# Performance work log

Measured on AMD Instinct MI355X. Metric: run time of the kernel, lower is better.

## Reference

```python
import jax, jax.numpy as jnp
import numpy as np

WS = 16         # window size
NH = 16         # num heads
EPS = 1e-6


def _ln(x):
    m = jnp.mean(x, axis=-1, keepdims=True)
    v = jnp.var(x, axis=-1, keepdims=True)
    return (x - m) * jax.lax.rsqrt(v + EPS)


def _modulate(x, shift, scale):
    return x * (1.0 + scale[:, None, :]) + shift[:, None, :]


def setup_inputs() -> dict:
    key = jax.random.key(0)
    ks = jax.random.split(key, 14)
    D, HD = 1024, 64
    s = 0.02
    return {
        'x': jax.random.normal(ks[0], (4, 4096, D), jnp.float32),
        'c': jax.random.normal(ks[1], (4, D), jnp.float32),
        'qkv_w': jax.random.normal(ks[2], (3 * D, D), jnp.float32) * s,
        'qkv_b': jax.random.normal(ks[3], (3 * D,), jnp.float32) * s,
        'proj_w': jax.random.normal(ks[4], (D, D), jnp.float32) * s,
        'proj_b': jax.random.normal(ks[5], (D,), jnp.float32) * s,
        'rel_pos_h': jax.random.normal(ks[6], (2 * WS - 1, HD), jnp.float32) * s,
        'rel_pos_w': jax.random.normal(ks[7], (2 * WS - 1, HD), jnp.float32) * s,
        'adaLN_w': jax.random.normal(ks[8], (6 * D, D), jnp.float32) * s,
        'adaLN_b': jax.random.normal(ks[9], (6 * D,), jnp.float32) * s,
        'fc1_w': jax.random.normal(ks[10], (4 * D, D), jnp.float32) * s,
        'fc1_b': jax.random.normal(ks[11], (4 * D,), jnp.float32) * s,
        'fc2_w': jax.random.normal(ks[12], (D, 4 * D), jnp.float32) * s,
        'fc2_b': jax.random.normal(ks[13], (D,), jnp.float32) * s,
    }


def _window_attention(x, qkv_w, qkv_b, proj_w, proj_b, rel_pos_h, rel_pos_w):
    # x: [N, T, D] with T = h*w, h = w = sqrt(T)
    N, T, D = x.shape
    h = w = int(round(T ** 0.5))
    nwh, nww = h // WS, w // WS  # grid divides evenly -> no padding
    hd = D // NH
    scale = hd ** -0.5

    # window partition: [N, h, w, D] -> [B, WS, WS, D], B = N*nwh*nww
    xw = x.reshape(N, nwh, WS, nww, WS, D).transpose(0, 1, 3, 2, 4, 5)
    xw = xw.reshape(N * nwh * nww, WS, WS, D)
    B = xw.shape[0]
    L = WS * WS

    qkv = (xw.reshape(B, L, D) @ qkv_w.T + qkv_b)  # [B, L, 3D]
    qkv = qkv.reshape(B, L, 3, NH, hd).transpose(2, 0, 3, 1, 4)  # [3, B, NH, L, hd]
    qkv = qkv.reshape(3, B * NH, L, hd)
    q, k, v = qkv[0], qkv[1], qkv[2]

    attn = jnp.einsum('bqc,bkc->bqk', q * scale, k)  # [B*NH, L, L]

    # decomposed relative position bias (q_size == k_size == WS)
    coords = jnp.arange(WS)
    rel_idx = coords[:, None] - coords[None, :] + (WS - 1)  # [WS, WS]
    Rh = rel_pos_h[rel_idx]  # [WS(q_h), WS(k_h), hd]
    Rw = rel_pos_w[rel_idx]  # [WS(q_w), WS(k_w), hd]
    rq = q.reshape(B * NH, WS, WS, hd)
    rel_h = jnp.einsum('bhwc,hkc->bhwk', rq, Rh)  # [B*NH, WS, WS, WS(kh)]
    rel_w = jnp.einsum('bhwc,wkc->bhwk', rq, Rw)  # [B*NH, WS, WS, WS(kw)]
    attn = (attn.reshape(B * NH, WS, WS, WS, WS)
            + rel_h[:, :, :, :, None]
            + rel_w[:, :, :, None, :]).reshape(B * NH, L, L)

    probs = jax.nn.softmax(attn, axis=-1)
    out = probs @ v  # [B*NH, L, hd]
    out = out.reshape(B, NH, WS, WS, hd).transpose(0, 2, 3, 1, 4).reshape(B, WS, WS, D)
    out = out @ proj_w.T + proj_b

    # window unpartition: [B, WS, WS, D] -> [N, T, D]
    out = out.reshape(N, nwh, nww, WS, WS, D).transpose(0, 1, 3, 2, 4, 5)
    return out.reshape(N, T, D)


def reference(x, c, qkv_w, qkv_b, proj_w, proj_b, rel_pos_h, rel_pos_w,
              adaLN_w, adaLN_b, fc1_w, fc1_b, fc2_w, fc2_b):
    D = x.shape[-1]
    mod = jax.nn.silu(c) @ adaLN_w.T + adaLN_b  # [N, 6D]
    sh_msa, sc_msa, g_msa, sh_mlp, sc_mlp, g_mlp = jnp.split(mod, 6, axis=1)

    a_in = _modulate(_ln(x), sh_msa, sc_msa)
    a_out = _window_attention(a_in, qkv_w, qkv_b, proj_w, proj_b, rel_pos_h, rel_pos_w)
    x = x + g_msa[:, None, :] * a_out

    m_in = _modulate(_ln(x), sh_mlp, sc_mlp)
    hdn = jax.nn.gelu(m_in @ fc1_w.T + fc1_b, approximate=True)
    m_out = hdn @ fc2_w.T + fc2_b
    x = x + g_mlp[:, None, :] * m_out
    return x
```

## Files before the change

### kernel.cpp

```cpp
#include <hip/hip_runtime.h>
#include <cstdint>
#include <cstddef>


typedef float  f32x4    __attribute__((ext_vector_type(4)));
typedef __bf16 bf16x8_t __attribute__((ext_vector_type(8)));
typedef __bf16 bf16x4_t __attribute__((ext_vector_type(4)));

#define DEV __device__ __forceinline__

DEV void gload_lds16(const void* g, void* l) {
    auto gp = (const uint32_t __attribute__((address_space(1)))*)(uintptr_t)g;
    auto lp = (uint32_t __attribute__((address_space(3)))*)(uint32_t)(uintptr_t)l;
    __builtin_amdgcn_global_load_lds(gp, lp, 16, 0, 0);
}

DEV bf16x8_t lds_frag(const __bf16* base, int row, int chunk, int row_elems) {
    return *(const bf16x8_t*)(base + row * row_elems + ((chunk ^ (row & 7)) << 3));
}

DEV bf16x8_t p_frag(const __bf16* base, int row, int chunk) {
    return *(const bf16x8_t*)(base + row * 32 + ((chunk ^ ((row >> 1) & 3)) << 3));
}

DEV int vt_addr(int d, int k) {
    return d * 64 + ((((k >> 3) ^ (d & 7) ^ ((d >> 3) & 7)) << 3) | (k & 7));
}

DEV float gelu_tanh(float v) {
    float u = 0.7978845608028654f * (v + 0.044715f * v * v * v);
    float e = __expf(2.f * u);
    float th = 1.f - 2.f / (e + 1.f);
    return 0.5f * v * (1.f + th);
}

DEV int win2tok(int r) {
    int nb = r >> 12, wi = (r >> 8) & 15, l = r & 255;
    return (nb << 12) + (wi >> 2) * 1024 + (l >> 4) * 64 + (wi & 3) * 16 + (l & 15);
}

__global__ void silu_k(const float* __restrict__ c, float* __restrict__ o, int n) {
    int i = blockIdx.x * 256 + threadIdx.x;
    if (i < n) { float v = c[i]; o[i] = v / (1.f + __expf(-v)); }
}

__global__ void zero_k(float* o, int n) {
    int i = blockIdx.x * 256 + threadIdx.x;
    if (i < n) o[i] = 0.f;
}

__global__ void conv_bf16(const float* __restrict__ s, __bf16* __restrict__ d, int n4) {
    int i = blockIdx.x * 256 + threadIdx.x;
    if (i < n4) {
        float4 v = ((const float4*)s)[i];
        bf16x4_t o; o[0] = (__bf16)v.x; o[1] = (__bf16)v.y; o[2] = (__bf16)v.z; o[3] = (__bf16)v.w;
        ((bf16x4_t*)d)[i] = o;
    }
}

__global__ __launch_bounds__(256)
void mod_gemv(const float* __restrict__ sc, const float* __restrict__ w,
              const float* __restrict__ b, float* __restrict__ mod) {
    int o = (blockIdx.x << 2) + (threadIdx.x >> 6);
    int lane = threadIdx.x & 63;
    int n = o / 6144, col = o % 6144;
    const float4* wr = (const float4*)(w + (size_t)col * 1024);
    const float4* sr = (const float4*)(sc + n * 1024);
    float acc = 0.f;
    #pragma unroll 4
    for (int i = lane; i < 256; i += 64) {
        float4 a = wr[i], x = sr[i];
        acc += a.x * x.x + a.y * x.y + a.z * x.z + a.w * x.w;
    }
    #pragma unroll
    for (int m = 1; m < 64; m <<= 1) acc += __shfl_xor(acc, m);
    if (lane == 0) mod[o] = acc + b[col];
}

__global__ __launch_bounds__(256)
void ln_mod_k(const float* __restrict__ src, const float* __restrict__ mod,
              int sh_off, int sc_off, __bf16* __restrict__ out, int permute, int r0) {
    int rl = blockIdx.x;
    int r = rl + r0;
    int nb = r >> 12;
    int t = permute ? win2tok(r) : r;
    float4 v = ((const float4*)(src + (size_t)t * 1024))[threadIdx.x];
    float s  = v.x + v.y + v.z + v.w;
    float sq = v.x * v.x + v.y * v.y + v.z * v.z + v.w * v.w;
    #pragma unroll
    for (int m = 1; m < 64; m <<= 1) { s += __shfl_xor(s, m); sq += __shfl_xor(sq, m); }
    __shared__ float ps[4], pq[4];
    int wv = threadIdx.x >> 6, ln = threadIdx.x & 63;
    if (ln == 0) { ps[wv] = s; pq[wv] = sq; }
    __syncthreads();
    s  = ps[0] + ps[1] + ps[2] + ps[3];
    sq = pq[0] + pq[1] + pq[2] + pq[3];
    float mean = s * (1.f / 1024.f);
    float var  = sq * (1.f / 1024.f) - mean * mean;
    float rstd = rsqrtf(var + 1e-6f);
    int c = threadIdx.x << 2;
    const float* mrow = mod + nb * 6144;
    float4 scv = *(const float4*)(mrow + sc_off + c);
    float4 shv = *(const float4*)(mrow + sh_off + c);
    bf16x4_t o;
    o[0] = (__bf16)((v.x - mean) * rstd * (1.f + scv.x) + shv.x);
    o[1] = (__bf16)((v.y - mean) * rstd * (1.f + scv.y) + shv.y);
    o[2] = (__bf16)((v.z - mean) * rstd * (1.f + scv.z) + shv.z);
    o[3] = (__bf16)((v.w - mean) * rstd * (1.f + scv.w) + shv.w);
    *(bf16x4_t*)(out + (size_t)rl * 1024 + c) = o;
}

template <int PM, int PN>
DEV void mfma16(f32x4 (&acc)[8][4], bf16x8_t (&fa)[4][2], bf16x8_t (&fb)[2][2][2]) {
    #pragma unroll
    for (int ks = 0; ks < 2; ++ks)
        #pragma unroll
        for (int mi = 0; mi < 4; ++mi)
            #pragma unroll
            for (int nn = 0; nn < 2; ++nn)
                acc[PM * 4 + mi][PN * 2 + nn] = __builtin_amdgcn_mfma_f32_16x16x32_bf16(
                    fa[mi][ks], fb[PN][nn][ks], acc[PM * 4 + mi][PN * 2 + nn], 0, 0, 0);
}

#define GBAR  __builtin_amdgcn_s_barrier()
#define PRIO1 __builtin_amdgcn_s_setprio(1)
#define PRIO0 __builtin_amdgcn_s_setprio(0)

template <int EPI>
__global__ __launch_bounds__(512)
void gemm256(const __bf16* __restrict__ A, const __bf16* __restrict__ B,
             const float* __restrict__ bias, void* __restrict__ Cout,
             const float* __restrict__ extra, const float* __restrict__ mod,
             int N, int K, int r0, int gx) {
    extern __shared__ __align__(16) char smem[];
    __bf16* lA = (__bf16*)smem;
    __bf16* lB = lA + 2 * 16384;
    const int tid = threadIdx.x, lane = tid & 63, wv = tid >> 6;
    const int wr = wv >> 2, wc = wv & 3;

    const int nwg = gridDim.x;
    const int qq = nwg >> 3, rr8 = nwg & 7;
    const int xcd = blockIdx.x & 7, pos = blockIdx.x >> 3;
    const int nid = (xcd < rr8 ? xcd * (qq + 1) : rr8 * (qq + 1) + (xcd - rr8) * qq) + pos;
    const int bm = (nid / gx) << 8, bn = (nid % gx) << 8;

    f32x4 acc[8][4];
    const f32x4 z4 = {0.f, 0.f, 0.f, 0.f};
    #pragma unroll
    for (int i = 0; i < 8; ++i)
        #pragma unroll
        for (int j = 0; j < 4; ++j) acc[i][j] = z4;

    bf16x8_t fa[4][2], fb[2][2][2];

    const int l8  = lane >> 3;
    const int gc8 = ((lane & 7) ^ l8) << 3;
    const int rbw = ((wv & 3) << 3) + ((wv >> 2) << 6);
    const __bf16* gA0 = A + (size_t)(bm +       (wv << 3) + l8) * K + gc8;
    const __bf16* gA1 = A + (size_t)(bm + 128 + (wv << 3) + l8) * K + gc8;
    const __bf16* gA2 = A + (size_t)(bm +  64 + (wv << 3) + l8) * K + gc8;
    const __bf16* gA3 = A + (size_t)(bm + 192 + (wv << 3) + l8) * K + gc8;
    const __bf16* gB0 = B + (size_t)(bn +       rbw + l8) * K + gc8;
    const __bf16* gB1 = B + (size_t)(bn + 128 + rbw + l8) * K + gc8;
    const __bf16* gB2 = B + (size_t)(bn +  32 + rbw + l8) * K + gc8;
    const __bf16* gB3 = B + (size_t)(bn + 160 + rbw + l8) * K + gc8;
    const int dA0 = (wv << 3) * 64, dA1 = (128 + (wv << 3)) * 64;
    const int dA2 = (64 + (wv << 3)) * 64, dA3 = (192 + (wv << 3)) * 64;
    const int dB0 = rbw * 64, dB1 = (128 + rbw) * 64;
    const int dB2 = (32 + rbw) * 64, dB3 = (160 + rbw) * 64;

    auto stageAll = [&](int be2) {
        gload_lds16(gA0, lA + be2 + dA0); gload_lds16(gA1, lA + be2 + dA1);
        gload_lds16(gB0, lB + be2 + dB0); gload_lds16(gB1, lB + be2 + dB1);
        gload_lds16(gB2, lB + be2 + dB2); gload_lds16(gB3, lB + be2 + dB3);
        gload_lds16(gA2, lA + be2 + dA2); gload_lds16(gA3, lA + be2 + dA3);
        gA0 += 64; gA1 += 64; gA2 += 64; gA3 += 64;
        gB0 += 64; gB1 += 64; gB2 += 64; gB3 += 64;
    };

    const int swzb = (lane >> 4) ^ (lane & 7);
    const __bf16* aR0 = lA + (wr << 13) + ((lane & 15) << 6) + (swzb << 3);
    const __bf16* aR1 = lA + (wr << 13) + ((lane & 15) << 6) + ((swzb ^ 4) << 3);
    const __bf16* bR0 = lB + (wc << 12) + ((lane & 15) << 6) + (swzb << 3);
    const __bf16* bR1 = lB + (wc << 12) + ((lane & 15) << 6) + ((swzb ^ 4) << 3);

    auto readA = [&](int be2, int pm) {
        #pragma unroll
        for (int mi = 0; mi < 4; ++mi) {
            fa[mi][0] = *(const bf16x8_t*)(aR0 + be2 + pm * 4096 + mi * 1024);
            fa[mi][1] = *(const bf16x8_t*)(aR1 + be2 + pm * 4096 + mi * 1024);
        }
    };
    auto readB = [&](int be2, int pn) {
        #pragma unroll
        for (int ni = 0; ni < 2; ++ni) {
            fb[pn][ni][0] = *(const bf16x8_t*)(bR0 + be2 + pn * 2048 + ni * 1024);
            fb[pn][ni][1] = *(const bf16x8_t*)(bR1 + be2 + pn * 2048 + ni * 1024);
        }
    };

    const int nt = K >> 6;
    stageAll(0);

    int be = 0;
    for (int t = 0; t < nt; ++t) {
        asm volatile("s_waitcnt vmcnt(0)" ::: "memory");
        GBAR;
        if (t + 1 < nt) stageAll(be ^ 16384);
        readA(be, 0); readB(be, 0); readB(be, 1);
        PRIO1; mfma16<0, 0>(acc, fa, fb); mfma16<0, 1>(acc, fa, fb); PRIO0;
        readA(be, 1);
        PRIO1; mfma16<1, 0>(acc, fa, fb); mfma16<1, 1>(acc, fa, fb); PRIO0;
        be ^= 16384;
    }

    #pragma unroll
    for (int am = 0; am < 8; ++am) {
        #pragma unroll
        for (int j = 0; j < 4; ++j) {
            int m = bm + (wr << 7) + (am << 4) + ((lane >> 4) << 2) + j;
            #pragma unroll
            for (int an = 0; an < 4; ++an) {
                int n = bn + (wc << 6) + (an << 4) + (lane & 15);
                float v = acc[am][an][j] + bias[n];
                if constexpr (EPI == 0) {
                    ((__bf16*)Cout)[(size_t)m * N + n] = (__bf16)v;
                } else if constexpr (EPI == 1) {
                    int mg = m + r0;
                    int tr = win2tok(mg);
                    float g = mod[(mg >> 12) * 6144 + 2048 + n];
                    ((float*)Cout)[(size_t)tr * 1024 + n] = extra[(size_t)tr * 1024 + n] + g * v;
                } else if constexpr (EPI == 2) {
                    ((__bf16*)Cout)[(size_t)m * N + n] = (__bf16)gelu_tanh(v);
                } else {
                    int mg = m + r0;
                    float g = mod[(mg >> 12) * 6144 + 5120 + n];
                    ((float*)Cout)[(size_t)mg * 1024 + n] = extra[(size_t)mg * 1024 + n] + g * v;
                }
            }
        }
    }
}

__global__ __launch_bounds__(256, 3)
void attn_k(const __bf16* __restrict__ qkv, const float* __restrict__ relh,
            const float* __restrict__ relw, __bf16* __restrict__ out) {
    __shared__ __align__(16) __bf16 lP[4][32 * 32];
    __shared__ __align__(16) __bf16 lKt[2][64 * 64];
    __shared__ __align__(16) __bf16 lVt[2][64 * 64];
    __shared__ __align__(16) __bf16 lTab[128 * 32];

    const int blk = blockIdx.x;
    const int winc = blk >> 5, h = (blk >> 1) & 15, qh = blk & 1;
    const int tid = threadIdx.x, lane = tid & 63, wv = tid >> 6;
    const __bf16* base = qkv + (size_t)winc * 256 * 3072 + h * 64;
    const int q0 = qh << 7;

    {
        __bf16* lR0 = lKt[0];
        __bf16* lR1 = lKt[1];
        for (int i = tid; i < 1984; i += 256) {
            int row = i >> 6, c = i & 63;
            lR0[row * 72 + c] = (__bf16)relh[i];
            lR1[row * 72 + c] = (__bf16)relw[i];
        }
    }
    __syncthreads();
    {
        const int r = tid >> 1, half = tid & 1;
        const int lwin = q0 + r;
        const int qi = lwin >> 4, qj = lwin & 15;
        const __bf16* qrow = base + (size_t)lwin * 3072;
        float ah[8], aw[8];
        #pragma unroll
        for (int kk = 0; kk < 8; ++kk) { ah[kk] = 0.f; aw[kk] = 0.f; }
        for (int c8 = 0; c8 < 8; ++c8) {
            bf16x8_t q8 = *(const bf16x8_t*)(qrow + (c8 << 3));
            float qf8[8];
            #pragma unroll
            for (int e = 0; e < 8; ++e) qf8[e] = (float)q8[e];
            #pragma unroll
            for (int kk = 0; kk < 8; ++kk) {
                int kg = (half << 3) + kk;
                bf16x8_t r1 = *(const bf16x8_t*)(lKt[0] + (qi - kg + 15) * 72 + (c8 << 3));
                bf16x8_t r2 = *(const bf16x8_t*)(lKt[1] + (qj - kg + 15) * 72 + (c8 << 3));
                float a1 = 0.f, a2 = 0.f;
                #pragma unroll
                for (int e = 0; e < 8; ++e) {
                    a1 += qf8[e] * (float)r1[e];
                    a2 += qf8[e] * (float)r2[e];
                }
                ah[kk] += a1; aw[kk] += a2;
            }
        }
        bf16x8_t oh, ow;
        #pragma unroll
        for (int kk = 0; kk < 8; ++kk) { oh[kk] = (__bf16)ah[kk]; ow[kk] = (__bf16)aw[kk]; }
        *(bf16x8_t*)(lTab + r * 32 + (half << 3))      = oh;
        *(bf16x8_t*)(lTab + r * 32 + 16 + (half << 3)) = ow;
    }
    __syncthreads();

    bf16x8_t qf[2][2];
    #pragma unroll
    for (int mi = 0; mi < 2; ++mi)
        #pragma unroll
        for (int ks = 0; ks < 2; ++ks) {
            int l = q0 + (wv << 5) + (mi << 4) + (lane & 15);
            qf[mi][ks] = *(const bf16x8_t*)(base + (size_t)l * 3072 + (((ks << 2) + (lane >> 4)) << 3));
        }
    {
        const __bf16* kb = base + 1024;
        #pragma unroll
        for (int q = 0; q < 2; ++q) {
            int c = (wv << 1) + q;
            int kl = (c << 3) + (lane >> 3);
            gload_lds16(kb + (size_t)kl * 3072 + (((lane & 7) ^ (lane >> 3)) << 3),
                        lKt[0] + c * 512);
        }
        const __bf16* vb = base + 2048;
        bf16x8_t a = *(const bf16x8_t*)(vb + (size_t)(tid >> 3) * 3072 + ((tid & 7) << 3));
        bf16x8_t b = *(const bf16x8_t*)(vb + (size_t)(32 + (tid >> 3)) * 3072 + ((tid & 7) << 3));
        int lc = tid & 7;
        #pragma unroll
        for (int e = 0; e < 8; ++e) {
            lVt[0][vt_addr(lc * 8 + e, tid >> 3)]        = a[e];
            lVt[0][vt_addr(lc * 8 + e, 32 + (tid >> 3))] = b[e];
        }
    }
    __syncthreads();

    float twv[2][4];
    #pragma unroll
    for (int mi = 0; mi < 2; ++mi)
        #pragma unroll
        for (int j = 0; j < 4; ++j) {
            int qr = (wv << 5) + (mi << 4) + ((lane >> 4) << 2) + j;
            twv[mi][j] = (float)lTab[qr * 32 + 16 + (lane & 15)];
        }

    const f32x4 z4 = {0.f, 0.f, 0.f, 0.f};
    f32x4 oacc[2][4];
    #pragma unroll
    for (int a = 0; a < 2; ++a)
        #pragma unroll
        for (int b = 0; b < 4; ++b) oacc[a][b] = z4;
    float rsum[2][4];
    #pragma unroll
    for (int a = 0; a < 2; ++a)
        #pragma unroll
        for (int j = 0; j < 4; ++j) rsum[a][j] = 0.f;
    __bf16* lPw = lP[wv];

    int cur = 0;
    for (int kt = 0; kt < 4; ++kt) {
        const bool pre = (kt < 3);
        bf16x8_t v8a, v8b;
        if (pre) {
            const __bf16* kb = base + 1024 + (size_t)(kt + 1) * 64 * 3072;
            #pragma unroll
            for (int q = 0; q < 2; ++q) {
                int c = (wv << 1) + q;
                int kl = (c << 3) + (lane >> 3);
                gload_lds16(kb + (size_t)kl * 3072 + (((lane & 7) ^ (lane >> 3)) << 3),
                            lKt[cur ^ 1] + c * 512);
            }
            const __bf16* vb = base + 2048 + (size_t)(kt + 1) * 64 * 3072;
            v8a = *(const bf16x8_t*)(vb + (size_t)(tid >> 3) * 3072 + ((tid & 7) << 3));
            v8b = *(const bf16x8_t*)(vb + (size_t)(32 + (tid >> 3)) * 3072 + ((tid & 7) << 3));
        }

        f32x4 s[2][4];
        #pragma unroll
        for (int a = 0; a < 2; ++a)
            #pragma unroll
            for (int b = 0; b < 4; ++b) s[a][b] = z4;
        #pragma unroll
        for (int ks = 0; ks < 2; ++ks) {
            bf16x8_t kf[4];
            #pragma unroll
            for (int ni = 0; ni < 4; ++ni)
                kf[ni] = lds_frag(lKt[cur], (ni << 4) + (lane & 15), (ks << 2) + (lane >> 4), 64);
            #pragma unroll
            for (int mi = 0; mi < 2; ++mi)
                #pragma unroll
                for (int ni = 0; ni < 4; ++ni)
                    s[mi][ni] = __builtin_amdgcn_mfma_f32_16x16x32_bf16(qf[mi][ks], kf[ni], s[mi][ni], 0, 0, 0);
        }

        #pragma unroll
        for (int mi = 0; mi < 2; ++mi) {
            #pragma unroll
            for (int j = 0; j < 4; ++j) {
                int qr = (wv << 5) + (mi << 4) + ((lane >> 4) << 2) + j;
                bf16x4_t th4 = *(const bf16x4_t*)(lTab + qr * 32 + (kt << 2));
                float rs = 0.f;
                #pragma unroll
                for (int ni = 0; ni < 4; ++ni) {
                    float p = __expf(s[mi][ni][j] * 0.125f + (float)th4[ni] + twv[mi][j]);
                    s[mi][ni][j] = p;
                    rs += p;
                }
                rsum[mi][j] += rs;
            }
        }

        #pragma unroll
        for (int hf = 0; hf < 2; ++hf) {
            #pragma unroll
            for (int mi = 0; mi < 2; ++mi) {
                #pragma unroll
                for (int j = 0; j < 4; ++j) {
                    int rl = (mi << 4) + ((lane >> 4) << 2) + j;
                    #pragma unroll
                    for (int b = 0; b < 2; ++b) {
                        int col = (b << 4) + (lane & 15);
                        lPw[rl * 32 + ((((col >> 3) ^ ((rl >> 1) & 3)) << 3) | (col & 7))] =
                            (__bf16)s[mi][(hf << 1) + b][j];
                    }
                }
            }
            bf16x8_t pf[2], vf[4];
            #pragma unroll
            for (int mi = 0; mi < 2; ++mi)
                pf[mi] = p_frag(lPw, (mi << 4) + (lane & 15), lane >> 4);
            #pragma unroll
            for (int no = 0; no < 4; ++no) {
                int d = (no << 4) + (lane & 15);
                vf[no] = *(const bf16x8_t*)(lVt[cur] + vt_addr(d, ((hf << 2) + (lane >> 4)) << 3));
            }
            #pragma unroll
            for (int mi = 0; mi < 2; ++mi)
                #pragma unroll
                for (int no = 0; no < 4; ++no)
                    oacc[mi][no] = __builtin_amdgcn_mfma_f32_16x16x32_bf16(pf[mi], vf[no], oacc[mi][no], 0, 0, 0);
        }

        if (pre) {
            int lc = tid & 7;
            #pragma unroll
            for (int e = 0; e < 8; ++e) {
                lVt[cur ^ 1][vt_addr(lc * 8 + e, tid >> 3)]        = v8a[e];
                lVt[cur ^ 1][vt_addr(lc * 8 + e, 32 + (tid >> 3))] = v8b[e];
            }
        }
        __syncthreads();
        cur ^= 1;
    }

    #pragma unroll
    for (int mi = 0; mi < 2; ++mi) {
        #pragma unroll
        for (int j = 0; j < 4; ++j) {
            float rs = rsum[mi][j];
            #pragma unroll
            for (int msk = 1; msk < 16; msk <<= 1) rs += __shfl_xor(rs, msk);
            float inv = 1.f / rs;
            int l = q0 + (wv << 5) + (mi << 4) + ((lane >> 4) << 2) + j;
            #pragma unroll
            for (int no = 0; no < 4; ++no) {
                int col = (no << 4) + (lane & 15);
                out[(size_t)(winc * 256 + l) * 1024 + h * 64 + col] = (__bf16)(oacc[mi][no][j] * inv);
            }
        }
    }
}

extern "C" void kernel_launch(void* const* d_in, const int* in_sizes, int n_in,
                              void* d_out, int out_size, void* d_ws, size_t ws_size,
                              hipStream_t stream) {
    const float* x      = (const float*)d_in[0];
    const float* c      = (const float*)d_in[1];
    const float* qkv_w  = (const float*)d_in[2];
    const float* qkv_b  = (const float*)d_in[3];
    const float* proj_w = (const float*)d_in[4];
    const float* proj_b = (const float*)d_in[5];
    const float* rel_h  = (const float*)d_in[6];
    const float* rel_w  = (const float*)d_in[7];
    const float* ada_w  = (const float*)d_in[8];
    const float* ada_b  = (const float*)d_in[9];
    const float* fc1_w  = (const float*)d_in[10];
    const float* fc1_b  = (const float*)d_in[11];
    const float* fc2_w  = (const float*)d_in[12];
    const float* fc2_b  = (const float*)d_in[13];
    float* xo = (float*)d_out;

    char* ws = (char*)d_ws;
    const size_t MB = 1ull << 20;
    int CH = 0;
    const int cands[7] = {16384, 8192, 4096, 2048, 1024, 512, 256};
    for (int i = 0; i < 7; ++i)
        if (26 * MB + (size_t)cands[i] * 10240 <= ws_size) { CH = cands[i]; break; }
    if (CH == 0) {
        zero_k<<<65536, 256, 0, stream>>>(xo, 16777216);
        return;
    }

    const int LDSB = 131072;
    hipFuncSetAttribute((const void*)&gemm256<0>, hipFuncAttributeMaxDynamicSharedMemorySize, LDSB);
    hipFuncSetAttribute((const void*)&gemm256<1>, hipFuncAttributeMaxDynamicSharedMemorySize, LDSB);
    hipFuncSetAttribute((const void*)&gemm256<2>, hipFuncAttributeMaxDynamicSharedMemorySize, LDSB);
    hipFuncSetAttribute((const void*)&gemm256<3>, hipFuncAttributeMaxDynamicSharedMemorySize, LDSB);

    const int NCH = 16384 / CH;
    float*  ws_silu = (float*)(ws);
    float*  ws_mod  = (float*)(ws + 65536);
    __bf16* w_qkv   = (__bf16*)(ws + 1 * MB);
    __bf16* w_proj  = (__bf16*)(ws + 7 * MB);
    __bf16* w_fc1   = (__bf16*)(ws + 9 * MB);
    __bf16* w_fc2   = (__bf16*)(ws + 17 * MB);
    __bf16* bufA    = (__bf16*)(ws + 26 * MB);
    __bf16* bufB    = (__bf16*)(ws + 26 * MB + (size_t)CH * 2048);

    silu_k   <<<16,   256, 0, stream>>>(c, ws_silu, 4096);
    mod_gemv <<<6144, 256, 0, stream>>>(ws_silu, ada_w, ada_b, ws_mod);
    conv_bf16<<<3072, 256, 0, stream>>>(qkv_w,  w_qkv,  786432);
    conv_bf16<<<1024, 256, 0, stream>>>(proj_w, w_proj, 262144);
    conv_bf16<<<4096, 256, 0, stream>>>(fc1_w,  w_fc1,  1048576);
    conv_bf16<<<4096, 256, 0, stream>>>(fc2_w,  w_fc2,  1048576);

    const int gy = CH / 256;
    for (int ci = 0; ci < NCH; ++ci) {
        int r0 = ci * CH;
        ln_mod_k<<<CH, 256, 0, stream>>>(x, ws_mod, 0, 1024, bufA, 1, r0);
        gemm256<0><<<12 * gy, 512, LDSB, stream>>>(bufA, w_qkv, qkv_b, bufB,
                                                   nullptr, nullptr, 3072, 1024, r0, 12);
        attn_k<<<(CH / 256) * 32, 256, 0, stream>>>(bufB, rel_h, rel_w, bufA);
        gemm256<1><<<4 * gy, 512, LDSB, stream>>>(bufA, w_proj, proj_b, xo,
                                                  x, ws_mod, 1024, 1024, r0, 4);
    }
    for (int ci = 0; ci < NCH; ++ci) {
        int r0 = ci * CH;
        ln_mod_k<<<CH, 256, 0, stream>>>(xo, ws_mod, 3072, 4096, bufA, 0, r0);
        gemm256<2><<<16 * gy, 512, LDSB, stream>>>(bufA, w_fc1, fc1_b, bufB,
                                                   nullptr, nullptr, 4096, 1024, r0, 16);
        gemm256<3><<<4 * gy, 512, LDSB, stream>>>(bufB, w_fc2, fc2_b, xo,
                                                  xo, ws_mod, 1024, 4096, r0, 4);
    }
}
```

Baseline: 630.3 us.

## Replace 256x256 GEMM tile with 128x128 tile, 8 waves, multi-block occupancy

Swaps the 256x256 output-tile GEMM for a 128x128 tile. Each of the 8 waves computes a 32x64 sub-tile, LDS use halves to 64KB, and launch bounds request several resident blocks per CU. The aim is more blocks per GEMM and better latency hiding through occupancy instead of large per-wave register tiles. The cost is lower operand reuse per LDS load and more global traffic per FLOP, and each wave now issues only 16 MFMAs per k-step, which may not cover load latency.

```diff
diff --git a/kernel.cpp b/kernel.cpp
--- a/kernel.cpp
+++ b/kernel.cpp
@@ -110,94 +110,57 @@
     *(bf16x4_t*)(out + (size_t)rl * 1024 + c) = o;
 }
 
-template <int PM, int PN>
-DEV void mfma16(f32x4 (&acc)[8][4], bf16x8_t (&fa)[4][2], bf16x8_t (&fb)[2][2][2]) {
-    #pragma unroll
-    for (int ks = 0; ks < 2; ++ks)
-        #pragma unroll
-        for (int mi = 0; mi < 4; ++mi)
-            #pragma unroll
-            for (int nn = 0; nn < 2; ++nn)
-                acc[PM * 4 + mi][PN * 2 + nn] = __builtin_amdgcn_mfma_f32_16x16x32_bf16(
-                    fa[mi][ks], fb[PN][nn][ks], acc[PM * 4 + mi][PN * 2 + nn], 0, 0, 0);
-}
-
 #define GBAR  __builtin_amdgcn_s_barrier()
 #define PRIO1 __builtin_amdgcn_s_setprio(1)
 #define PRIO0 __builtin_amdgcn_s_setprio(0)
 
 template <int EPI>
-__global__ __launch_bounds__(512)
-void gemm256(const __bf16* __restrict__ A, const __bf16* __restrict__ B,
-             const float* __restrict__ bias, void* __restrict__ Cout,
-             const float* __restrict__ extra, const float* __restrict__ mod,
-             int N, int K, int r0, int gx) {
+__global__ __launch_bounds__(512, 4)
+void gemmw8(const __bf16* __restrict__ A, const __bf16* __restrict__ B,
+            const float* __restrict__ bias, void* __restrict__ Cout,
+            const float* __restrict__ extra, const float* __restrict__ mod,
+            int N, int K, int r0, int gx) {
     extern __shared__ __align__(16) char smem[];
     __bf16* lA = (__bf16*)smem;
-    __bf16* lB = lA + 2 * 16384;
+    __bf16* lB = lA + 2 * 8192;
     const int tid = threadIdx.x, lane = tid & 63, wv = tid >> 6;
-    const int wr = wv >> 2, wc = wv & 3;
+    const int wr = wv >> 1, wc = wv & 1;
 
     const int nwg = gridDim.x;
     const int qq = nwg >> 3, rr8 = nwg & 7;
     const int xcd = blockIdx.x & 7, pos = blockIdx.x >> 3;
     const int nid = (xcd < rr8 ? xcd * (qq + 1) : rr8 * (qq + 1) + (xcd - rr8) * qq) + pos;
-    const int bm = (nid / gx) << 8, bn = (nid % gx) << 8;
-
-    f32x4 acc[8][4];
+    const int bm = (nid / gx) << 7, bn = (nid % gx) << 7;
+
+    f32x4 acc[2][4];
     const f32x4 z4 = {0.f, 0.f, 0.f, 0.f};
     #pragma unroll
-    for (int i = 0; i < 8; ++i)
+    for (int i = 0; i < 2; ++i)
         #pragma unroll
         for (int j = 0; j < 4; ++j) acc[i][j] = z4;
 
-    bf16x8_t fa[4][2], fb[2][2][2];
+    bf16x8_t fa[2][2], fb[4][2];
 
     const int l8  = lane >> 3;
     const int gc8 = ((lane & 7) ^ l8) << 3;
-    const int rbw = ((wv & 3) << 3) + ((wv >> 2) << 6);
-    const __bf16* gA0 = A + (size_t)(bm +       (wv << 3) + l8) * K + gc8;
-    const __bf16* gA1 = A + (size_t)(bm + 128 + (wv << 3) + l8) * K + gc8;
-    const __bf16* gA2 = A + (size_t)(bm +  64 + (wv << 3) + l8) * K + gc8;
-    const __bf16* gA3 = A + (size_t)(bm + 192 + (wv << 3) + l8) * K + gc8;
-    const __bf16* gB0 = B + (size_t)(bn +       rbw + l8) * K + gc8;
-    const __bf16* gB1 = B + (size_t)(bn + 128 + rbw + l8) * K + gc8;
-    const __bf16* gB2 = B + (size_t)(bn +  32 + rbw + l8) * K + gc8;
-    const __bf16* gB3 = B + (size_t)(bn + 160 + rbw + l8) * K + gc8;
-    const int dA0 = (wv << 3) * 64, dA1 = (128 + (wv << 3)) * 64;
-    const int dA2 = (64 + (wv << 3)) * 64, dA3 = (192 + (wv << 3)) * 64;
-    const int dB0 = rbw * 64, dB1 = (128 + rbw) * 64;
-    const int dB2 = (32 + rbw) * 64, dB3 = (160 + rbw) * 64;
+    const int rw  = (wv << 4) + l8;
+    const __bf16* gA0 = A + (size_t)(bm + rw)     * K + gc8;
+    const __bf16* gA1 = A + (size_t)(bm + rw + 8) * K + gc8;
+    const __bf16* gB0 = B + (size_t)(bn + rw)     * K + gc8;
+    const __bf16* gB1 = B + (size_t)(bn + rw + 8) * K + gc8;
+    const int d0 = (wv << 4) * 64, d1 = ((wv << 4) + 8) * 64;
 
     auto stageAll = [&](int be2) {
-        gload_lds16(gA0, lA + be2 + dA0); gload_lds16(gA1, lA + be2 + dA1);
-        gload_lds16(gB0, lB + be2 + dB0); gload_lds16(gB1, lB + be2 + dB1);
-        gload_lds16(gB2, lB + be2 + dB2); gload_lds16(gB3, lB + be2 + dB3);
-        gload_lds16(gA2, lA + be2 + dA2); gload_lds16(gA3, lA + be2 + dA3);
-        gA0 += 64; gA1 += 64; gA2 += 64; gA3 += 64;
-        gB0 += 64; gB1 += 64; gB2 += 64; gB3 += 64;
+        gload_lds16(gA0, lA + be2 + d0); gload_lds16(gA1, lA + be2 + d1);
+        gload_lds16(gB0, lB + be2 + d0); gload_lds16(gB1, lB + be2 + d1);
+        gA0 += 64; gA1 += 64; gB0 += 64; gB1 += 64;
     };
 
     const int swzb = (lane >> 4) ^ (lane & 7);
-    const __bf16* aR0 = lA + (wr << 13) + ((lane & 15) << 6) + (swzb << 3);
-    const __bf16* aR1 = lA + (wr << 13) + ((lane & 15) << 6) + ((swzb ^ 4) << 3);
+    const __bf16* aR0 = lA + (wr << 11) + ((lane & 15) << 6) + (swzb << 3);
+    const __bf16* aR1 = lA + (wr << 11) + ((lane & 15) << 6) + ((swzb ^ 4) << 3);
     const __bf16* bR0 = lB + (wc << 12) + ((lane & 15) << 6) + (swzb << 3);
     const __bf16* bR1 = lB + (wc << 12) + ((lane & 15) << 6) + ((swzb ^ 4) << 3);
-
-    auto readA = [&](int be2, int pm) {
-        #pragma unroll
-        for (int mi = 0; mi < 4; ++mi) {
-            fa[mi][0] = *(const bf16x8_t*)(aR0 + be2 + pm * 4096 + mi * 1024);
-            fa[mi][1] = *(const bf16x8_t*)(aR1 + be2 + pm * 4096 + mi * 1024);
-        }
-    };
-    auto readB = [&](int be2, int pn) {
-        #pragma unroll
-        for (int ni = 0; ni < 2; ++ni) {
-            fb[pn][ni][0] = *(const bf16x8_t*)(bR0 + be2 + pn * 2048 + ni * 1024);
-            fb[pn][ni][1] = *(const bf16x8_t*)(bR1 + be2 + pn * 2048 + ni * 1024);
-        }
-    };
 
     const int nt = K >> 6;
     stageAll(0);
@@ -206,23 +169,39 @@
     for (int t = 0; t < nt; ++t) {
         asm volatile("s_waitcnt vmcnt(0)" ::: "memory");
         GBAR;
-        if (t + 1 < nt) stageAll(be ^ 16384);
-        readA(be, 0); readB(be, 0); readB(be, 1);
-        PRIO1; mfma16<0, 0>(acc, fa, fb); mfma16<0, 1>(acc, fa, fb); PRIO0;
-        readA(be, 1);
-        PRIO1; mfma16<1, 0>(acc, fa, fb); mfma16<1, 1>(acc, fa, fb); PRIO0;
-        be ^= 16384;
-    }
-
-    #pragma unroll
-    for (int am = 0; am < 8; ++am) {
+        if (t + 1 < nt) stageAll(be ^ 8192);
+        #pragma unroll
+        for (int mi = 0; mi < 2; ++mi) {
+            fa[mi][0] = *(const bf16x8_t*)(aR0 + be + mi * 1024);
+            fa[mi][1] = *(const bf16x8_t*)(aR1 + be + mi * 1024);
+        }
+        #pragma unroll
+        for (int ni = 0; ni < 4; ++ni) {
+            fb[ni][0] = *(const bf16x8_t*)(bR0 + be + ni * 1024);
+            fb[ni][1] = *(const bf16x8_t*)(bR1 + be + ni * 1024);
+        }
+        PRIO1;
+        #pragma unroll
+        for (int ks = 0; ks < 2; ++ks)
+            #pragma unroll
+            for (int mi = 0; mi < 2; ++mi)
+                #pragma unroll
+                for (int ni = 0; ni < 4; ++ni)
+                    acc[mi][ni] = __builtin_amdgcn_mfma_f32_16x16x32_bf16(
+                        fa[mi][ks], fb[ni][ks], acc[mi][ni], 0, 0, 0);
+        PRIO0;
+        be ^= 8192;
+    }
+
+    #pragma unroll
+    for (int mi = 0; mi < 2; ++mi) {
         #pragma unroll
         for (int j = 0; j < 4; ++j) {
-            int m = bm + (wr << 7) + (am << 4) + ((lane >> 4) << 2) + j;
-            #pragma unroll
-            for (int an = 0; an < 4; ++an) {
-                int n = bn + (wc << 6) + (an << 4) + (lane & 15);
-                float v = acc[am][an][j] + bias[n];
+            int m = bm + (wr << 5) + (mi << 4) + ((lane >> 4) << 2) + j;
+            #pragma unroll
+            for (int ni = 0; ni < 4; ++ni) {
+                int n = bn + (wc << 6) + (ni << 4) + (lane & 15);
+                float v = acc[mi][ni][j] + bias[n];
                 if constexpr (EPI == 0) {
                     ((__bf16*)Cout)[(size_t)m * N + n] = (__bf16)v;
                 } else if constexpr (EPI == 1) {
@@ -496,11 +475,11 @@
         return;
     }
 
-    const int LDSB = 131072;
-    hipFuncSetAttribute((const void*)&gemm256<0>, hipFuncAttributeMaxDynamicSharedMemorySize, LDSB);
-    hipFuncSetAttribute((const void*)&gemm256<1>, hipFuncAttributeMaxDynamicSharedMemorySize, LDSB);
-    hipFuncSetAttribute((const void*)&gemm256<2>, hipFuncAttributeMaxDynamicSharedMemorySize, LDSB);
-    hipFuncSetAttribute((const void*)&gemm256<3>, hipFuncAttributeMaxDynamicSharedMemorySize, LDSB);
+    const int LDSB = 65536;
+    hipFuncSetAttribute((const void*)&gemmw8<0>, hipFuncAttributeMaxDynamicSharedMemorySize, LDSB);
+    hipFuncSetAttribute((const void*)&gemmw8<1>, hipFuncAttributeMaxDynamicSharedMemorySize, LDSB);
+    hipFuncSetAttribute((const void*)&gemmw8<2>, hipFuncAttributeMaxDynamicSharedMemorySize, LDSB);
+    hipFuncSetAttribute((const void*)&gemmw8<3>, hipFuncAttributeMaxDynamicSharedMemorySize, LDSB);
 
     const int NCH = 16384 / CH;
     float*  ws_silu = (float*)(ws);
@@ -519,22 +498,22 @@
     conv_bf16<<<4096, 256, 0, stream>>>(fc1_w,  w_fc1,  1048576);
     conv_bf16<<<4096, 256, 0, stream>>>(fc2_w,  w_fc2,  1048576);
 
-    const int gy = CH / 256;
+    const int gy = CH / 128;
     for (int ci = 0; ci < NCH; ++ci) {
         int r0 = ci * CH;
         ln_mod_k<<<CH, 256, 0, stream>>>(x, ws_mod, 0, 1024, bufA, 1, r0);
-        gemm256<0><<<12 * gy, 512, LDSB, stream>>>(bufA, w_qkv, qkv_b, bufB,
-                                                   nullptr, nullptr, 3072, 1024, r0, 12);
+        gemmw8<0><<<24 * gy, 512, LDSB, stream>>>(bufA, w_qkv, qkv_b, bufB,
+                                                  nullptr, nullptr, 3072, 1024, r0, 24);
         attn_k<<<(CH / 256) * 32, 256, 0, stream>>>(bufB, rel_h, rel_w, bufA);
-        gemm256<1><<<4 * gy, 512, LDSB, stream>>>(bufA, w_proj, proj_b, xo,
-                                                  x, ws_mod, 1024, 1024, r0, 4);
+        gemmw8<1><<<8 * gy, 512, LDSB, stream>>>(bufA, w_proj, proj_b, xo,
+                                                 x, ws_mod, 1024, 1024, r0, 8);
     }
     for (int ci = 0; ci < NCH; ++ci) {
         int r0 = ci * CH;
         ln_mod_k<<<CH, 256, 0, stream>>>(xo, ws_mod, 3072, 4096, bufA, 0, r0);
-        gemm256<2><<<16 * gy, 512, LDSB, stream>>>(bufA, w_fc1, fc1_b, bufB,
-                                                   nullptr, nullptr, 4096, 1024, r0, 16);
-        gemm256<3><<<4 * gy, 512, LDSB, stream>>>(bufB, w_fc2, fc2_b, xo,
-                                                  xo, ws_mod, 1024, 4096, r0, 4);
-    }
-}
+        gemmw8<2><<<32 * gy, 512, LDSB, stream>>>(bufA, w_fc1, fc1_b, bufB,
+                                                  nullptr, nullptr, 4096, 1024, r0, 32);
+        gemmw8<3><<<8 * gy, 512, LDSB, stream>>>(bufB, w_fc2, fc2_b, xo,
+                                                 xo, ws_mod, 1024, 4096, r0, 8);
+    }
+}
```

New measurement: 677.6 us. 1.08x slower.
